# Kernel optimization log

Hardware: AMD Instinct MI355X
Metric: run time of the kernel (lower is better)

The kernel has to match this reference:

```python
import jax, jax.numpy as jnp
import numpy as np

B, T, D, H = 512, 200, 128, 128


def setup_inputs() -> dict:
    key = jax.random.key(0)
    ks = jax.random.split(key, 16)
    r = lambda k, shp, s=0.05: jax.random.normal(k, shp, dtype=jnp.float32) * s
    F = 3 * D + H  # concat([item_eb, his_sum, item_eb*his_sum, final_state2])
    return {
        "item_eb": jax.random.normal(ks[0], (B, D), dtype=jnp.float32),
        "item_his_eb": jax.random.normal(ks[1], (B, T, D), dtype=jnp.float32),
        "Wg1": r(ks[2], (D + H, 2 * H)), "bg1": jnp.ones((2 * H,), jnp.float32),
        "Wc1": r(ks[3], (D + H, H)), "bc1": jnp.zeros((H,), jnp.float32),
        "att_w1": r(ks[4], (4 * H, 80)), "att_b1": jnp.zeros((80,), jnp.float32),
        "att_w2": r(ks[5], (80, 40)), "att_b2": jnp.zeros((40,), jnp.float32),
        "att_w3": r(ks[6], (40, 1)), "att_b3": jnp.zeros((1,), jnp.float32),
        "Wg2": r(ks[7], (2 * H, 2 * H)), "bg2": jnp.ones((2 * H,), jnp.float32),
        "Wc2": r(ks[8], (2 * H, H)), "bc2": jnp.zeros((H,), jnp.float32),
        "fc1_w": r(ks[9], (F, 200)), "fc1_b": jnp.zeros((200,), jnp.float32),
        "alpha1": jnp.full((200,), 0.25, jnp.float32),
        "fc2_w": r(ks[10], (200, 80)), "fc2_b": jnp.zeros((80,), jnp.float32),
        "alpha2": jnp.full((80,), 0.25, jnp.float32),
        "fc3_w": r(ks[11], (80, 2)), "fc3_b": jnp.zeros((2,), jnp.float32),
        "seq_len": jax.random.randint(ks[12], (B,), 1, T + 1).astype(jnp.int32),
    }


def _gru_scan(x_btd, Wg, bg, Wc, bc, seq_len, att=None):
    """GRU (TF GRUCell math) or AUGRU if att [B,T] is given.
    Honors sequence_length semantics of tf dynamic_rnn: state copied through,
    outputs zeroed past each row's length."""
    Bx, Tx, _ = x_btd.shape
    Hh = Wc.shape[1]
    xs = jnp.swapaxes(x_btd, 0, 1)  # [T,B,Din]
    ts = jnp.arange(Tx)
    a_ts = jnp.swapaxes(att, 0, 1) if att is not None else jnp.zeros((Tx, Bx), x_btd.dtype)
    h0 = jnp.zeros((Bx, Hh), x_btd.dtype)

    def step(h, xat):
        x, a, t = xat
        gates = jax.nn.sigmoid(jnp.concatenate([x, h], axis=-1) @ Wg + bg)
        rg, u = jnp.split(gates, 2, axis=-1)
        c = jnp.tanh(jnp.concatenate([x, rg * h], axis=-1) @ Wc + bc)
        if att is not None:  # VecAttGRUCell: u = (1 - att_score) * u
            u = (1.0 - a[:, None]) * u
        hn = u * h + (1.0 - u) * c
        valid = (t < seq_len)[:, None]
        hn = jnp.where(valid, hn, h)
        out = jnp.where(valid, hn, jnp.zeros_like(hn))
        return hn, out

    hT, outs = jax.lax.scan(step, h0, (xs, a_ts, ts))
    return jnp.swapaxes(outs, 0, 1), hT  # [B,T,H], [B,H]


def _forward(item_eb, item_his_eb, Wg1, bg1, Wc1, bc1, att_w1, att_b1, att_w2, att_b2,
             att_w3, att_b3, Wg2, bg2, Wc2, bc2, fc1_w, fc1_b, alpha1, fc2_w, fc2_b,
             alpha2, fc3_w, fc3_b, seq_len):
    Bx, Tx, Dx = item_his_eb.shape
    mask = jnp.arange(Tx)[None, :] < seq_len[:, None]  # [B,T] bool
    # rnn_1: plain GRU over history embeddings
    rnn1, _ = _gru_scan(item_his_eb, Wg1, bg1, Wc1, bc1, seq_len)
    # din_fcn_attention: concat trick + 3-layer scorer + masked softmax
    q = jnp.broadcast_to(item_eb[:, None, :], rnn1.shape)
    din_all = jnp.concatenate([q, rnn1, q - rnn1, q * rnn1], axis=-1)  # [B,T,4H]
    h1 = jax.nn.sigmoid(din_all @ att_w1 + att_b1)
    h2 = jax.nn.sigmoid(h1 @ att_w2 + att_b2)
    scores = (h2 @ att_w3 + att_b3)[..., 0]  # [B,T]
    NEG_INF = jnp.float32(-(2.0 ** 32) + 1.0)  # DIEN padding value
    scores = jnp.where(mask, scores, NEG_INF)
    alphas = jax.nn.softmax(scores, axis=-1)  # [B,T]
    # rnn_2: AUGRU (VecAttGRUCell) gated by attention scores; take final state
    _, final_state2 = _gru_scan(rnn1, Wg2, bg2, Wc2, bc2, seq_len, att=alphas)
    # fcn head on concatenated features
    his_sum = jnp.sum(item_his_eb * mask[..., None].astype(item_his_eb.dtype), axis=1)
    feat = jnp.concatenate([item_eb, his_sum, item_eb * his_sum, final_state2], axis=-1)
    prelu = lambda x, a: jnp.maximum(x, 0.0) + a * jnp.minimum(x, 0.0)
    z = prelu(feat @ fc1_w + fc1_b, alpha1)
    z = prelu(z @ fc2_w + fc2_b, alpha2)
    logits = z @ fc3_w + fc3_b  # [B,2]
    return jax.nn.softmax(logits, axis=-1)


def reference(item_eb, item_his_eb, Wg1, bg1, Wc1, bc1, att_w1, att_b1, att_w2, att_b2,
              att_w3, att_b3, Wg2, bg2, Wc2, bc2, fc1_w, fc1_b, alpha1, fc2_w, fc2_b,
              alpha2, fc3_w, fc3_b, seq_len):
    return _forward(item_eb, item_his_eb, Wg1, bg1, Wc1, bc1, att_w1, att_b1, att_w2,
                    att_b2, att_w3, att_b3, Wg2, bg2, Wc2, bc2, fc1_w, fc1_b, alpha1,
                    fc2_w, fc2_b, alpha2, fc3_w, fc3_b, seq_len)
```

## Files before the change

### kernel.cpp

```cpp
#include <hip/hip_runtime.h>
#include <hip/hip_bf16.h>


typedef __attribute__((ext_vector_type(8))) short bf16x8;
typedef __attribute__((ext_vector_type(4))) float f32x4;
typedef _Float16 f16x2 __attribute__((ext_vector_type(2)));

#define NC 4
#define TC 50
#define CROWS 25600
#define CSH 3276800

static __device__ __forceinline__ unsigned short f2bf(float f) {
  union { __hip_bfloat16 h; unsigned short u; } v;
  v.h = __float2bfloat16(f);
  return v.u;
}
static __device__ __forceinline__ float bf2f(unsigned short u) {
  union { __hip_bfloat16 h; unsigned short u; } v;
  v.u = u;
  return __bfloat162float(v.h);
}
static __device__ __forceinline__ unsigned short f2h(float f) {
  union { _Float16 h; unsigned short u; } v;
  v.h = (_Float16)f;
  return v.u;
}
static __device__ __forceinline__ float h2f(unsigned short u) {
  union { unsigned short u; _Float16 h; } v;
  v.u = u;
  return (float)v.h;
}
static __device__ __forceinline__ unsigned int pkf16(float a, float b) {
  union { f16x2 v; unsigned int u; } c;
  c.v = (f16x2){(_Float16)a, (_Float16)b};
  return c.u;
}
static __device__ __forceinline__ void dot2a(float& acc, unsigned int w, unsigned int h) {
  asm volatile("v_dot2_f32_f16 %0, %1, %2, %0" : "+v"(acc) : "v"(w), "v"(h));
}
static __device__ __forceinline__ void gbar() {
  __builtin_amdgcn_sched_barrier(0);
  asm volatile("s_waitcnt lgkmcnt(0)" ::: "memory");
  __builtin_amdgcn_s_barrier();
  __builtin_amdgcn_sched_barrier(0);
}

__global__ __launch_bounds__(256) void prep_weights(
    const float* __restrict__ item_eb,
    const float* __restrict__ Wg1, const float* __restrict__ Wc1,
    const float* __restrict__ Wg2, const float* __restrict__ Wc2,
    const float* __restrict__ aw1, const float* __restrict__ aw2,
    const float* __restrict__ aw3,
    const float* __restrict__ bg1, const float* __restrict__ bc1,
    const float* __restrict__ bg2, const float* __restrict__ bc2,
    const float* __restrict__ ab1, const float* __restrict__ ab2,
    unsigned short* __restrict__ W1xT, unsigned short* __restrict__ W2xT,
    unsigned short* __restrict__ AW1T, unsigned short* __restrict__ AW2T,
    float* __restrict__ b384_1, float* __restrict__ b384_2,
    float* __restrict__ bA1, float* __restrict__ bA2,
    unsigned int* __restrict__ WgP1, unsigned int* __restrict__ WcP1,
    unsigned int* __restrict__ WgP2, unsigned int* __restrict__ WcP2,
    float* __restrict__ w3p, unsigned short* __restrict__ Xq,
    float* __restrict__ hstate)
{
  int e = blockIdx.x * 256 + threadIdx.x;
  if (e < 49152) {
    int n = e >> 7, k = e & 127;
    float v1 = (n < 256) ? Wg1[k * 256 + n] : Wc1[k * 128 + (n - 256)];
    float v2 = (n < 256) ? Wg2[k * 256 + n] : Wc2[k * 128 + (n - 256)];
    W1xT[e] = f2bf(v1);
    W2xT[e] = f2bf(v2);
  }
  if (e < 65536) {
    int n = e >> 9, k = e & 511;
    AW1T[e] = f2bf(n < 80 ? aw1[k * 80 + n] : 0.f);
    Xq[e] = f2bf(item_eb[e]);
    hstate[e] = 0.f;
  }
  if (e < 16384) {
    int n = e >> 7, k = e & 127;
    AW2T[e] = f2bf((n < 40 && k < 80) ? aw2[k * 40 + n] : 0.f);
  }
  if (e < 16384) {
    int i = e >> 8, tt = e & 255;
    int row = 128 + 2 * i;
    WgP1[e] = pkf16(Wg1[row * 256 + tt], Wg1[(row + 1) * 256 + tt]);
    WgP2[e] = pkf16(Wg2[row * 256 + tt], Wg2[(row + 1) * 256 + tt]);
  }
  if (e < 8192) {
    int i = e >> 8, tt = e & 255;
    int jc = tt >> 1, half = tt & 1;
    int row = 128 + half * 64 + 2 * i;
    WcP1[e] = pkf16(Wc1[row * 128 + jc], Wc1[(row + 1) * 128 + jc]);
    WcP2[e] = pkf16(Wc2[row * 128 + jc], Wc2[(row + 1) * 128 + jc]);
  }
  if (e < 384) {
    b384_1[e] = (e < 256) ? bg1[e] : bc1[e - 256];
    b384_2[e] = (e < 256) ? bg2[e] : bc2[e - 256];
  }
  if (e < 128) {
    bA1[e] = (e < 80) ? ab1[e] : 0.f;
    bA2[e] = (e < 40) ? ab2[e] : 0.f;
    w3p[e] = (e < 40) ? aw3[e] : 0.f;
  }
}

__global__ __launch_bounds__(256) void cast_his_t(const float4* __restrict__ in4,
                                                  ushort4* __restrict__ out4)
{
  int i = blockIdx.x * 256 + threadIdx.x;
  float4 v = in4[i];
  int d4 = (i & 31) << 2;
  int bt = i >> 5;
  int tt = bt % 200, bb = bt / 200;
  out4[(((size_t)tt * 512 + bb) * 128 + d4) >> 2] =
      make_ushort4(f2bf(v.x), f2bf(v.y), f2bf(v.z), f2bf(v.w));
}

struct GemmP {
  const unsigned short* A;
  const unsigned short* B;
  const float* bias;
  unsigned short* out;
  float* scores;
  const float* w3p;
  const float* b3;
  const unsigned short* Xq;
  const unsigned short* rnn1;
  long rowbase;
  int K, ldc, mtiles, tbase;
};

static __device__ __forceinline__ uint4 bfop(uint4 q, uint4 r, bool mul) {
  unsigned short* qs = (unsigned short*)&q;
  unsigned short* rs = (unsigned short*)&r;
  uint4 o;
  unsigned short* os = (unsigned short*)&o;
#pragma unroll
  for (int i = 0; i < 8; i++) {
    float a = bf2f(qs[i]), b = bf2f(rs[i]);
    os[i] = f2bf(mul ? a * b : a - b);
  }
  return o;
}

template <int SRC, int EPI>
__device__ __forceinline__ void gemm_body(const GemmP& P, int tile, char* smem) {
// ... 64 lines not shown
  if (EPI == 2) {
    float sp[2][4] = {{0.f, 0.f, 0.f, 0.f}, {0.f, 0.f, 0.f, 0.f}};
#pragma unroll
    for (int n = 0; n < 8; n++) {
      int gcol = n * 16 + lcol;
      float bb = P.bias[gcol];
      float w3 = P.w3p[gcol];
#pragma unroll
      for (int m = 0; m < 2; m++)
#pragma unroll
        for (int i = 0; i < 4; i++) {
          float v = acc[m][n][i] + bb;
          sp[m][i] += w3 / (1.f + __expf(-v));
        }
    }
#pragma unroll
    for (int msk = 1; msk < 16; msk <<= 1)
#pragma unroll
      for (int m = 0; m < 2; m++)
#pragma unroll
        for (int i = 0; i < 4; i++) sp[m][i] += __shfl_xor(sp[m][i], msk);
    float b3v = P.b3[0];
    if (lcol == 0) {
#pragma unroll
      for (int m = 0; m < 2; m++)
#pragma unroll
        for (int i = 0; i < 4; i++) {
          long grow = mBase + w * 32 + m * 16 + lrow4 + i;
          int b = (int)(grow & 511);
          int tp = (int)(grow >> 9) + P.tbase;
          P.scores[b * 200 + tp] = sp[m][i] + b3v;
        }
    }
  } else {
#pragma unroll
    for (int n = 0; n < 8; n++) {
      int gcol = nBase + n * 16 + lcol;
      float bb = P.bias[gcol];
#pragma unroll
      for (int m = 0; m < 2; m++)
#pragma unroll
        for (int i = 0; i < 4; i++) {
          long grow = mBase + w * 32 + m * 16 + lrow4 + i;
          float v = acc[m][n][i] + bb;
          if (EPI == 0) P.out[grow * P.ldc + gcol] = f2h(v);
          else          P.out[grow * P.ldc + gcol] = f2bf(1.f / (1.f + __expf(-v)));
        }
    }
  }
}

struct GruP {
  const unsigned short* xproj;
  const unsigned int* WgP;
  const unsigned int* WcP;
  const int* seqlen;
  const float* alphas;
  unsigned short* outbf;
  float* hstate;
  int tbase;
};

template <int AUGRU>
__device__ void gru_body(const GruP& P, int r, char* smem) {
  float* hF = (float*)smem;
  float* uF = hF + 128;
  unsigned int* hH = (unsigned int*)(uF + 128);
  unsigned int* rghP = hH + 64;
  const int t = threadIdx.x;
  const int jc = t >> 1;
  const int len = P.seqlen[r];
  int nsteps = len - P.tbase;
  if (nsteps > TC) nsteps = TC;

  if (nsteps <= 0) {
    if (!AUGRU && t < 64) {
      for (int s = 0; s < TC; s++)
        ((unsigned int*)(P.outbf + ((size_t)(P.tbase + s) * 512 + r) * 128))[t] = 0;
    }
    return;
  }
  __builtin_amdgcn_s_setprio(1);

  unsigned int wg[64], wc[32];
#pragma unroll
  for (int i = 0; i < 64; i++) wg[i] = P.WgP[i * 256 + t];
#pragma unroll
  for (int i = 0; i < 32; i++) wc[i] = P.WcP[i * 256 + t];

  if (t < 128) hF[t] = P.hstate[r * 128 + t];
  if (t < 64) hH[t] = pkf16(P.hstate[r * 128 + 2 * t], P.hstate[r * 128 + 2 * t + 1]);
  gbar();

  const unsigned short* xp = P.xproj;
  const size_t RS = (size_t)512 * 384;
  const size_t base = (size_t)r * 384;
  unsigned short gA = xp[base + t], cA = xp[base + 256 + jc];
  int s1 = nsteps > 1 ? 1 : 0;
  unsigned short gB = xp[s1 * RS + base + t], cB = xp[s1 * RS + base + 256 + jc];
  float alA = AUGRU ? P.alphas[r * 200 + P.tbase] : 0.f;
  float alB = AUGRU ? P.alphas[r * 200 + P.tbase + s1] : 0.f;

  for (int ts = 0; ts < nsteps; ++ts) {
    int tsn = (ts + 2 < nsteps) ? ts + 2 : nsteps - 1;
    size_t off = (size_t)tsn * RS + base;
    unsigned short gC = xp[off + t];
    unsigned short cC = xp[off + 256 + jc];
    float alC = AUGRU ? P.alphas[r * 200 + P.tbase + tsn] : 0.f;

    float a0 = 0.f, a1 = 0.f, a2 = 0.f, a3 = 0.f;
#pragma unroll
    for (int q = 0; q < 4; q++) {
      uint4 h0 = *(const uint4*)&hH[q * 16 + 0];
      uint4 h1 = *(const uint4*)&hH[q * 16 + 4];
      uint4 h2 = *(const uint4*)&hH[q * 16 + 8];
      uint4 h3 = *(const uint4*)&hH[q * 16 + 12];
      dot2a(a0, wg[q * 16 + 0], h0.x);  dot2a(a1, wg[q * 16 + 1], h0.y);
      dot2a(a2, wg[q * 16 + 2], h0.z);  dot2a(a3, wg[q * 16 + 3], h0.w);
      dot2a(a0, wg[q * 16 + 4], h1.x);  dot2a(a1, wg[q * 16 + 5], h1.y);
      dot2a(a2, wg[q * 16 + 6], h1.z);  dot2a(a3, wg[q * 16 + 7], h1.w);
      dot2a(a0, wg[q * 16 + 8], h2.x);  dot2a(a1, wg[q * 16 + 9], h2.y);
      dot2a(a2, wg[q * 16 + 10], h2.z); dot2a(a3, wg[q * 16 + 11], h2.w);
      dot2a(a0, wg[q * 16 + 12], h3.x); dot2a(a1, wg[q * 16 + 13], h3.y);
      dot2a(a2, wg[q * 16 + 14], h3.z); dot2a(a3, wg[q * 16 + 15], h3.w);
    }
    float a = (a0 + a1) + (a2 + a3) + h2f(gA);
    float g = 1.f / (1.f + __expf(-a));
    if (t < 128) {
      float rgh = g * hF[t];
      float rh2 = __shfl_down(rgh, 1);
      if (!(t & 1)) rghP[t >> 1] = pkf16(rgh, rh2);
    } else {
      uF[t - 128] = g;
    }
    gbar();

    float c0 = 0.f, c1 = 0.f;
    const uint4* rp = (const uint4*)&rghP[(t & 1) * 32];
#pragma unroll
    for (int q = 0; q < 8; q++) {
      uint4 rq = rp[q];
      dot2a(c0, wc[q * 4 + 0], rq.x);
      dot2a(c1, wc[q * 4 + 1], rq.y);
      dot2a(c0, wc[q * 4 + 2], rq.z);
      dot2a(c1, wc[q * 4 + 3], rq.w);
    }
    float c = c0 + c1;
    c += __shfl_xor(c, 1);
    c += h2f(cA);
    c = fminf(fmaxf(c, -15.f), 15.f);
    float e2 = __expf(2.f * c);
    c = 1.f - 2.f / (e2 + 1.f);
    float u = uF[jc];
    if (AUGRU) u *= (1.f - alA);
    float h = hF[jc];
    float hn = u * h + (1.f - u) * c;
    float hnHi = __shfl_down(hn, 2);
    if (!(t & 1)) {
      hF[jc] = hn;
      if (!AUGRU) P.outbf[((size_t)(P.tbase + ts) * 512 + r) * 128 + jc] = f2bf(hn);
    }
    if (!(t & 3)) hH[t >> 2] = pkf16(hn, hnHi);
    gbar();

    gA = gB; cA = cB; alA = alB;
    gB = gC; cB = cC; alB = alC;
  }

  if (t < 128) P.hstate[r * 128 + t] = hF[t];
  if (!AUGRU && nsteps < TC && t < 64) {
    for (int s = nsteps; s < TC; s++)
      ((unsigned int*)(P.outbf + ((size_t)(P.tbase + s) * 512 + r) * 128))[t] = 0;
  }
}

__device__ void hsum_body(const float* __restrict__ his, float* __restrict__ hs,
                          const int* __restrict__ seqlen, int b, char* smem) {
  float* sm = (float*)smem;
  int t = threadIdx.x;
  int len = seqlen[b];
  int col = t & 127, hf = t >> 7;
  float s = 0.f;
  for (int ts = hf; ts < len; ts += 2) s += his[((size_t)b * 200 + ts) * 128 + col];
  sm[t] = s;
  __syncthreads();
  if (t < 128) hs[b * 128 + t] = sm[t] + sm[t + 128];
}

template <int AUG, int GRU, int S1, int E1, int S2, int E2, int S3, int E3, int HS>
__global__ __launch_bounds__(256) void fatk(GruP gp, GemmP p1, int c1,
                                            GemmP p2, int c2, GemmP p3,
                                            const float* hisp, float* hsp)
{
  extern __shared__ char smem[];
  int id = blockIdx.x;
  if constexpr (GRU) {
    if (id < 512) { gru_body<AUG>(gp, id, smem); return; }
    id -= 512;
  }
  if constexpr (HS) {
    if (id < 512) { hsum_body(hisp, hsp, gp.seqlen, id, smem); return; }
    id -= 512;
  }
  if constexpr (S1 >= 0) {
    if (id < c1) { gemm_body<S1, E1>(p1, id, smem); return; }
    id -= c1;
  }
  if constexpr (S2 >= 0) {
    if (id < c2) { gemm_body<S2, E2>(p2, id, smem); return; }
    id -= c2;
  }
  if constexpr (S3 >= 0) gemm_body<S3, E3>(p3, id, smem);
}

__global__ __launch_bounds__(256) void mask_softmax(
    const float* __restrict__ scores, const int* __restrict__ seqlen,
    float* __restrict__ alphas, float* __restrict__ hstate)
{
  int b = blockIdx.x, t = threadIdx.x;
  __shared__ float red[256];
  if (t < 128) hstate[b * 128 + t] = 0.f;
  int len = seqlen[b];
  float s = (t < 200 && t < len) ? scores[b * 200 + t] : -1e30f;
  red[t] = s;
  __syncthreads();
  for (int o = 128; o > 0; o >>= 1) {
    if (t < o) red[t] = fmaxf(red[t], red[t + o]);
    __syncthreads();
  }
  float m = red[0];
  __syncthreads();
  float e = (t < 200 && t < len) ? __expf(s - m) : 0.f;
  red[t] = e;
  __syncthreads();
  for (int o = 128; o > 0; o >>= 1) {
    if (t < o) red[t] += red[t + o];
    __syncthreads();
  }
  float denom = red[0];
  if (t < 200) alphas[b * 200 + t] = e / denom;
}

__global__ __launch_bounds__(256) void head_kernel(
    const float* __restrict__ item_eb, const float* __restrict__ hs,
    const float* __restrict__ hstate,
    const float* __restrict__ w1, const float* __restrict__ b1, const float* __restrict__ a1,
    const float* __restrict__ w2, const float* __restrict__ b2, const float* __restrict__ a2,
    const float* __restrict__ w3, const float* __restrict__ b3,
    float* __restrict__ out)
{
  int b = blockIdx.x, t = threadIdx.x;
// ... 25 lines not shown
  __syncthreads();
  if (t == 0) {
    float l0 = b3[0], l1 = b3[1];
    for (int k = 0; k < 80; k++) {
      float z = z2[k];
      l0 += z * w3[k * 2];
      l1 += z * w3[k * 2 + 1];
    }
    float m = fmaxf(l0, l1);
    float e0 = __expf(l0 - m), e1 = __expf(l1 - m);
    out[b * 2 + 0] = e0 / (e0 + e1);
    out[b * 2 + 1] = e1 / (e0 + e1);
  }
}

extern "C" void kernel_launch(void* const* d_in, const int* in_sizes, int n_in,
                              void* d_out, int out_size, void* d_ws, size_t ws_size,
                              hipStream_t stream)
{
  const float* item_eb = (const float*)d_in[0];
  const float* his     = (const float*)d_in[1];
  const float* Wg1     = (const float*)d_in[2];
  const float* bg1     = (const float*)d_in[3];
  const float* Wc1     = (const float*)d_in[4];
  const float* bc1     = (const float*)d_in[5];
  const float* aw1     = (const float*)d_in[6];
  const float* ab1     = (const float*)d_in[7];
  const float* aw2     = (const float*)d_in[8];
  const float* ab2     = (const float*)d_in[9];
  const float* aw3     = (const float*)d_in[10];
  const float* ab3     = (const float*)d_in[11];
  const float* Wg2     = (const float*)d_in[12];
  const float* bg2     = (const float*)d_in[13];
  const float* Wc2     = (const float*)d_in[14];
  const float* bc2     = (const float*)d_in[15];
  const float* fc1w    = (const float*)d_in[16];
  const float* fc1b    = (const float*)d_in[17];
  const float* al1     = (const float*)d_in[18];
  const float* fc2w    = (const float*)d_in[19];
  const float* fc2b    = (const float*)d_in[20];
  const float* al2     = (const float*)d_in[21];
  const float* fc3w    = (const float*)d_in[22];
  const float* fc3b    = (const float*)d_in[23];
  const int*   seqlen  = (const int*)d_in[24];

  char* ws = (char*)d_ws;
  unsigned short* XhA    = (unsigned short*)(ws + 0L);
  unsigned short* xpA    = (unsigned short*)(ws + 26214400L);
  unsigned short* xpB    = (unsigned short*)(ws + 45875200L);
  unsigned short* rnn1   = (unsigned short*)(ws + 65536000L);
  float*          scores = (float*)(ws + 91750400L);
  float*          alphas = (float*)(ws + 92160000L);
  float*          hstate = (float*)(ws + 92569600L);
  unsigned int*   WgP1   = (unsigned int*)(ws + 92831744L);
  unsigned int*   WcP1   = (unsigned int*)(ws + 92897280L);
  unsigned int*   WgP2   = (unsigned int*)(ws + 92930048L);
  unsigned int*   WcP2   = (unsigned int*)(ws + 92995584L);
  unsigned short* W1xT   = (unsigned short*)(ws + 93028352L);
  unsigned short* W2xT   = (unsigned short*)(ws + 93126656L);
  unsigned short* AW1T   = (unsigned short*)(ws + 93224960L);
  unsigned short* AW2T   = (unsigned short*)(ws + 93356032L);
  float*          b384_1 = (float*)(ws + 93388800L);
  float*          b384_2 = (float*)(ws + 93390336L);
  float*          bA1    = (float*)(ws + 93391872L);
  float*          bA2    = (float*)(ws + 93392384L);
  float*          w3p    = (float*)(ws + 93392896L);
  unsigned short* Xq     = (unsigned short*)(ws + 93393408L);
  float*          hs     = scores;

  unsigned short* h1[NC] = {XhA, XhA + CSH, XhA + 2 * CSH, XhA + 3 * CSH};

  const int SM = 32768;
  GruP gz{}; GemmP dz{};
  gz.seqlen = seqlen;

  auto mkGru = [&](int c, int aug) {
    GruP g;
    g.xproj = (c & 1) ? xpB : xpA;
    g.WgP = aug ? WgP2 : WgP1; g.WcP = aug ? WcP2 : WcP1;
    g.seqlen = seqlen; g.alphas = alphas;
    g.outbf = aug ? nullptr : rnn1; g.hstate = hstate; g.tbase = c * TC;
    return g;
  };
  auto mkXp = [&](const unsigned short* A, const float* bias, unsigned short* outp) {
    GemmP p{}; p.A = A; p.B = (bias == b384_1) ? W1xT : W2xT; p.bias = bias;
    p.out = outp; p.K = 128; p.ldc = 384; p.mtiles = 200; return p;
  };
  auto mkAtt1 = [&](int c) {
    GemmP p{}; p.B = AW1T; p.bias = bA1; p.out = h1[c];
    p.Xq = Xq; p.rnn1 = rnn1; p.rowbase = (long)c * CROWS;
    p.K = 512; p.ldc = 128; p.mtiles = 200; return p;
  };
  auto mkAtt2 = [&](int c) {
    GemmP p{}; p.A = h1[c]; p.B = AW2T; p.bias = bA2;
    p.scores = scores; p.w3p = w3p; p.b3 = ab3;
    p.K = 128; p.ldc = 128; p.mtiles = 200; p.tbase = c * TC; return p;
  };

  prep_weights<<<256, 256, 0, stream>>>(item_eb, Wg1, Wc1, Wg2, Wc2, aw1, aw2, aw3,
                                        bg1, bc1, bg2, bc2, ab1, ab2,
                                        W1xT, W2xT, AW1T, AW2T, b384_1, b384_2, bA1, bA2,
                                        WgP1, WcP1, WgP2, WcP2, w3p, Xq, hstate);
  cast_his_t<<<12800, 256, 0, stream>>>((const float4*)his, (ushort4*)XhA);

  fatk<0,0, 0,0, -1,0, -1,0, 0><<<600, 256, SM, stream>>>(
      gz, mkXp(XhA, b384_1, xpA), 600, dz, 0, dz, nullptr, nullptr);
  fatk<0,1, 0,0, -1,0, -1,0, 0><<<1112, 256, SM, stream>>>(
      mkGru(0,0), mkXp(XhA + (size_t)CSH, b384_1, xpB), 600, dz, 0, dz, nullptr, nullptr);
  fatk<0,1, 0,0, -1,0, -1,0, 0><<<1112, 256, SM, stream>>>(
      mkGru(1,0), mkXp(XhA + (size_t)2*CSH, b384_1, xpA), 600, dz, 0, dz, nullptr, nullptr);
  fatk<0,1, 0,0, 1,1, -1,0, 0><<<1712, 256, SM, stream>>>(
      mkGru(2,0), mkXp(XhA + (size_t)3*CSH, b384_1, xpB), 600, mkAtt1(0), 200, dz, nullptr, nullptr);
  fatk<0,1, 1,1, 0,2, -1,0, 0><<<912, 256, SM, stream>>>(
      mkGru(3,0), mkAtt1(1), 200, mkAtt2(0), 200, dz, nullptr, nullptr);
  fatk<0,0, 1,1, 0,2, 0,0, 0><<<1000, 256, SM, stream>>>(
      gz, mkAtt1(2), 200, mkAtt2(1), 200, mkXp(rnn1, b384_2, xpA), nullptr, nullptr);
  fatk<0,0, 1,1, 0,2, 0,0, 0><<<1000, 256, SM, stream>>>(
      gz, mkAtt1(3), 200, mkAtt2(2), 200, mkXp(rnn1 + (size_t)CSH, b384_2, xpB), nullptr, nullptr);
  fatk<0,0, 0,2, -1,0, -1,0, 0><<<200, 256, SM, stream>>>(
      gz, mkAtt2(3), 200, dz, 0, dz, nullptr, nullptr);
  mask_softmax<<<512, 256, 0, stream>>>(scores, seqlen, alphas, hstate);
  fatk<1,1, -1,0, -1,0, -1,0, 1><<<1024, 256, SM, stream>>>(
      mkGru(0,1), dz, 0, dz, 0, dz, his, hs);
  fatk<1,1, 0,0, -1,0, -1,0, 0><<<1112, 256, SM, stream>>>(
      mkGru(1,1), mkXp(rnn1 + (size_t)2*CSH, b384_2, xpA), 600, dz, 0, dz, nullptr, nullptr);
  fatk<1,1, 0,0, -1,0, -1,0, 0><<<1112, 256, SM, stream>>>(
      mkGru(2,1), mkXp(rnn1 + (size_t)3*CSH, b384_2, xpB), 600, dz, 0, dz, nullptr, nullptr);
  fatk<1,1, -1,0, -1,0, -1,0, 0><<<512, 256, SM, stream>>>(
      mkGru(3,1), dz, 0, dz, 0, dz, nullptr, nullptr);
  head_kernel<<<512, 256, 0, stream>>>(item_eb, hs, hstate,
                                       fc1w, fc1b, al1, fc2w, fc2b, al2,
                                       fc3w, fc3b, (float*)d_out);
}
```

Measured before the change: 664.2 us.

## Batch GRU recurrence 16 rows per block using f16 MFMA instead of dot2

Replaces the per-row GRU blocks (512 blocks, each doing one hidden-state matvec with v_dot2 and registers-held packed weights) with 32 blocks that each process 16 batch rows, computing the h·W gate and candidate products with 16x16x32 f16 MFMA from a swizzled LDS tile. Weights are re-laid out as transposed f16 matrices. Sequence-length masking moves to per-row select inside a block that runs to the max length of its 16 rows. This cuts the number of GRU workgroups and their weight-register loading, freeing CUs for the fused GEMM work. The cost is serialized per-step latency concentrated in only 32 blocks and wasted steps for shorter rows.

```diff
diff --git a/kernel.cpp b/kernel.cpp
--- a/kernel.cpp
+++ b/kernel.cpp
@@ -4,12 +4,13 @@
 
 typedef __attribute__((ext_vector_type(8))) short bf16x8;
 typedef __attribute__((ext_vector_type(4))) float f32x4;
-typedef _Float16 f16x2 __attribute__((ext_vector_type(2)));
+typedef _Float16 f16x8 __attribute__((ext_vector_type(8)));
 
 #define NC 4
 #define TC 50
 #define CROWS 25600
 #define CSH 3276800
+#define NGRU 32
 
 static __device__ __forceinline__ unsigned short f2bf(float f) {
   union { __hip_bfloat16 h; unsigned short u; } v;
@@ -30,14 +31,6 @@
   union { unsigned short u; _Float16 h; } v;
   v.u = u;
   return (float)v.h;
-}
-static __device__ __forceinline__ unsigned int pkf16(float a, float b) {
-  union { f16x2 v; unsigned int u; } c;
-  c.v = (f16x2){(_Float16)a, (_Float16)b};
-  return c.u;
-}
-static __device__ __forceinline__ void dot2a(float& acc, unsigned int w, unsigned int h) {
-  asm volatile("v_dot2_f32_f16 %0, %1, %2, %0" : "+v"(acc) : "v"(w), "v"(h));
 }
 static __device__ __forceinline__ void gbar() {
   __builtin_amdgcn_sched_barrier(0);
@@ -59,8 +52,8 @@
     unsigned short* __restrict__ AW1T, unsigned short* __restrict__ AW2T,
     float* __restrict__ b384_1, float* __restrict__ b384_2,
     float* __restrict__ bA1, float* __restrict__ bA2,
-    unsigned int* __restrict__ WgP1, unsigned int* __restrict__ WcP1,
-    unsigned int* __restrict__ WgP2, unsigned int* __restrict__ WcP2,
+    unsigned short* __restrict__ WghT1, unsigned short* __restrict__ WchT1,
+    unsigned short* __restrict__ WghT2, unsigned short* __restrict__ WchT2,
     float* __restrict__ w3p, unsigned short* __restrict__ Xq,
     float* __restrict__ hstate)
 {
@@ -82,18 +75,15 @@
     int n = e >> 7, k = e & 127;
     AW2T[e] = f2bf((n < 40 && k < 80) ? aw2[k * 40 + n] : 0.f);
   }
+  if (e < 32768) {
+    int n = e >> 7, k = e & 127;
+    WghT1[e] = f2h(Wg1[(128 + k) * 256 + n]);
+    WghT2[e] = f2h(Wg2[(128 + k) * 256 + n]);
+  }
   if (e < 16384) {
-    int i = e >> 8, tt = e & 255;
-    int row = 128 + 2 * i;
-    WgP1[e] = pkf16(Wg1[row * 256 + tt], Wg1[(row + 1) * 256 + tt]);
-    WgP2[e] = pkf16(Wg2[row * 256 + tt], Wg2[(row + 1) * 256 + tt]);
-  }
-  if (e < 8192) {
-    int i = e >> 8, tt = e & 255;
-    int jc = tt >> 1, half = tt & 1;
-    int row = 128 + half * 64 + 2 * i;
-    WcP1[e] = pkf16(Wc1[row * 128 + jc], Wc1[(row + 1) * 128 + jc]);
-    WcP2[e] = pkf16(Wc2[row * 128 + jc], Wc2[(row + 1) * 128 + jc]);
+    int n = e >> 7, k = e & 127;
+    WchT1[e] = f2h(Wc1[(128 + k) * 128 + n]);
+    WchT2[e] = f2h(Wc2[(128 + k) * 128 + n]);
   }
   if (e < 384) {
     b384_1[e] = (e < 256) ? bg1[e] : bc1[e - 256];
@@ -264,8 +254,8 @@
 
 struct GruP {
   const unsigned short* xproj;
-  const unsigned int* WgP;
-  const unsigned int* WcP;
+  const unsigned short* Wgh;
+  const unsigned short* Wch;
   const int* seqlen;
   const float* alphas;
   unsigned short* outbf;
@@ -273,116 +263,161 @@
   int tbase;
 };
 
+static __device__ __forceinline__ int swz(int row, int colByte) {
+  return row * 256 + (colByte ^ ((row & 7) << 4));
+}
+
 template <int AUGRU>
-__device__ void gru_body(const GruP& P, int r, char* smem) {
-  float* hF = (float*)smem;
-  float* uF = hF + 128;
-  unsigned int* hH = (unsigned int*)(uF + 128);
-  unsigned int* rghP = hH + 64;
+__device__ void gru_body(const GruP& P, int rblk, char* smem) {
   const int t = threadIdx.x;
-  const int jc = t >> 1;
-  const int len = P.seqlen[r];
-  int nsteps = len - P.tbase;
-  if (nsteps > TC) nsteps = TC;
-
-  if (nsteps <= 0) {
-    if (!AUGRU && t < 64) {
-      for (int s = 0; s < TC; s++)
-        ((unsigned int*)(P.outbf + ((size_t)(P.tbase + s) * 512 + r) * 128))[t] = 0;
+  const int w = t >> 6, l = t & 63;
+  const int lo = l & 15, hi = l >> 4;
+  const int b0 = rblk * 16;
+
+  int mlen = 0;
+#pragma unroll
+  for (int i = 0; i < 16; i++) mlen = max(mlen, P.seqlen[b0 + i]);
+  int bsteps = mlen - P.tbase;
+  if (bsteps > TC) bsteps = TC;
+
+  if (bsteps <= 0) {
+    if (!AUGRU) {
+      for (int s = 0; s < TC; s++) {
+        unsigned int* zp = (unsigned int*)(P.outbf + ((size_t)(P.tbase + s) * 512 + b0) * 128);
+        for (int e = t; e < 1024; e += 256) zp[e] = 0;
+      }
     }
     return;
   }
   __builtin_amdgcn_s_setprio(1);
 
-  unsigned int wg[64], wc[32];
-#pragma unroll
-  for (int i = 0; i < 64; i++) wg[i] = P.WgP[i * 256 + t];
-#pragma unroll
-  for (int i = 0; i < 32; i++) wc[i] = P.WcP[i * 256 + t];
-
-  if (t < 128) hF[t] = P.hstate[r * 128 + t];
-  if (t < 64) hH[t] = pkf16(P.hstate[r * 128 + 2 * t], P.hstate[r * 128 + 2 * t + 1]);
+  int len[4];
+#pragma unroll
+  for (int i = 0; i < 4; i++) len[i] = P.seqlen[b0 + hi * 4 + i];
+
+  f16x8 wg[4][4], wc[2][4];
+#pragma unroll
+  for (int n = 0; n < 4; n++) {
+    int nt = w + n * 4;
+#pragma unroll
+    for (int ck = 0; ck < 4; ck++)
+      wg[n][ck] = *(const f16x8*)(P.Wgh + (nt * 16 + lo) * 128 + ck * 32 + hi * 8);
+  }
+#pragma unroll
+  for (int n = 0; n < 2; n++) {
+    int nt = w + n * 4;
+#pragma unroll
+    for (int ck = 0; ck < 4; ck++)
+      wc[n][ck] = *(const f16x8*)(P.Wch + (nt * 16 + lo) * 128 + ck * 32 + hi * 8);
+  }
+
+  char* hL = smem;
+  char* rL = smem + 4096;
+
+  const int colc0 = w * 16 + lo, colc1 = 64 + w * 16 + lo;
+  float hreg[2][4];
+#pragma unroll
+  for (int i = 0; i < 4; i++) {
+    int row = hi * 4 + i;
+    float h0 = P.hstate[(b0 + row) * 128 + colc0];
+    float h1 = P.hstate[(b0 + row) * 128 + colc1];
+    hreg[0][i] = h0;
+    hreg[1][i] = h1;
+    *(unsigned short*)(hL + swz(row, colc0 * 2)) = f2h(h0);
+    *(unsigned short*)(hL + swz(row, colc1 * 2)) = f2h(h1);
+  }
   gbar();
 
   const unsigned short* xp = P.xproj;
   const size_t RS = (size_t)512 * 384;
-  const size_t base = (size_t)r * 384;
-  unsigned short gA = xp[base + t], cA = xp[base + 256 + jc];
-  int s1 = nsteps > 1 ? 1 : 0;
-  unsigned short gB = xp[s1 * RS + base + t], cB = xp[s1 * RS + base + 256 + jc];
-  float alA = AUGRU ? P.alphas[r * 200 + P.tbase] : 0.f;
-  float alB = AUGRU ? P.alphas[r * 200 + P.tbase + s1] : 0.f;
-
-  for (int ts = 0; ts < nsteps; ++ts) {
-    int tsn = (ts + 2 < nsteps) ? ts + 2 : nsteps - 1;
-    size_t off = (size_t)tsn * RS + base;
-    unsigned short gC = xp[off + t];
-    unsigned short cC = xp[off + 256 + jc];
-    float alC = AUGRU ? P.alphas[r * 200 + P.tbase + tsn] : 0.f;
-
-    float a0 = 0.f, a1 = 0.f, a2 = 0.f, a3 = 0.f;
-#pragma unroll
-    for (int q = 0; q < 4; q++) {
-      uint4 h0 = *(const uint4*)&hH[q * 16 + 0];
-      uint4 h1 = *(const uint4*)&hH[q * 16 + 4];
-      uint4 h2 = *(const uint4*)&hH[q * 16 + 8];
-      uint4 h3 = *(const uint4*)&hH[q * 16 + 12];
-      dot2a(a0, wg[q * 16 + 0], h0.x);  dot2a(a1, wg[q * 16 + 1], h0.y);
-      dot2a(a2, wg[q * 16 + 2], h0.z);  dot2a(a3, wg[q * 16 + 3], h0.w);
-      dot2a(a0, wg[q * 16 + 4], h1.x);  dot2a(a1, wg[q * 16 + 5], h1.y);
-      dot2a(a2, wg[q * 16 + 6], h1.z);  dot2a(a3, wg[q * 16 + 7], h1.w);
-      dot2a(a0, wg[q * 16 + 8], h2.x);  dot2a(a1, wg[q * 16 + 9], h2.y);
-      dot2a(a2, wg[q * 16 + 10], h2.z); dot2a(a3, wg[q * 16 + 11], h2.w);
-      dot2a(a0, wg[q * 16 + 12], h3.x); dot2a(a1, wg[q * 16 + 13], h3.y);
-      dot2a(a2, wg[q * 16 + 14], h3.z); dot2a(a3, wg[q * 16 + 15], h3.w);
-    }
-    float a = (a0 + a1) + (a2 + a3) + h2f(gA);
-    float g = 1.f / (1.f + __expf(-a));
-    if (t < 128) {
-      float rgh = g * hF[t];
-      float rh2 = __shfl_down(rgh, 1);
-      if (!(t & 1)) rghP[t >> 1] = pkf16(rgh, rh2);
-    } else {
-      uF[t - 128] = g;
+
+  for (int ts = 0; ts < bsteps; ++ts) {
+    unsigned short xgs[4][4], xcs[2][4];
+    float al[4];
+#pragma unroll
+    for (int i = 0; i < 4; i++) {
+      size_t rb = (size_t)ts * RS + (size_t)(b0 + hi * 4 + i) * 384;
+      xgs[0][i] = xp[rb + 16 * w + lo];
+      xgs[1][i] = xp[rb + 64 + 16 * w + lo];
+      xgs[2][i] = xp[rb + 128 + 16 * w + lo];
+      xgs[3][i] = xp[rb + 192 + 16 * w + lo];
+      xcs[0][i] = xp[rb + 256 + 16 * w + lo];
+      xcs[1][i] = xp[rb + 320 + 16 * w + lo];
+      if (AUGRU) al[i] = P.alphas[(b0 + hi * 4 + i) * 200 + P.tbase + ts];
+    }
+
+    f16x8 aF[4];
+#pragma unroll
+    for (int ck = 0; ck < 4; ck++)
+      aF[ck] = *(const f16x8*)(hL + swz(lo, ck * 64 + hi * 16));
+    f32x4 acc1[4];
+#pragma unroll
+    for (int n = 0; n < 4; n++) {
+      acc1[n] = 0.f;
+#pragma unroll
+      for (int ck = 0; ck < 4; ck++)
+        acc1[n] = __builtin_amdgcn_mfma_f32_16x16x32_f16(aF[ck], wg[n][ck], acc1[n], 0, 0, 0);
+    }
+    float uu[2][4];
+#pragma unroll
+    for (int i = 0; i < 4; i++) {
+      int row = hi * 4 + i;
+      float r0 = 1.f / (1.f + __expf(-(acc1[0][i] + h2f(xgs[0][i]))));
+      float r1 = 1.f / (1.f + __expf(-(acc1[1][i] + h2f(xgs[1][i]))));
+      *(unsigned short*)(rL + swz(row, colc0 * 2)) = f2h(r0 * hreg[0][i]);
+      *(unsigned short*)(rL + swz(row, colc1 * 2)) = f2h(r1 * hreg[1][i]);
+      uu[0][i] = 1.f / (1.f + __expf(-(acc1[2][i] + h2f(xgs[2][i]))));
+      uu[1][i] = 1.f / (1.f + __expf(-(acc1[3][i] + h2f(xgs[3][i]))));
     }
     gbar();
 
-    float c0 = 0.f, c1 = 0.f;
-    const uint4* rp = (const uint4*)&rghP[(t & 1) * 32];
-#pragma unroll
-    for (int q = 0; q < 8; q++) {
-      uint4 rq = rp[q];
-      dot2a(c0, wc[q * 4 + 0], rq.x);
-      dot2a(c1, wc[q * 4 + 1], rq.y);
-      dot2a(c0, wc[q * 4 + 2], rq.z);
-      dot2a(c1, wc[q * 4 + 3], rq.w);
-    }
-    float c = c0 + c1;
-    c += __shfl_xor(c, 1);
-    c += h2f(cA);
-    c = fminf(fmaxf(c, -15.f), 15.f);
-    float e2 = __expf(2.f * c);
-    c = 1.f - 2.f / (e2 + 1.f);
-    float u = uF[jc];
-    if (AUGRU) u *= (1.f - alA);
-    float h = hF[jc];
-    float hn = u * h + (1.f - u) * c;
-    float hnHi = __shfl_down(hn, 2);
-    if (!(t & 1)) {
-      hF[jc] = hn;
-      if (!AUGRU) P.outbf[((size_t)(P.tbase + ts) * 512 + r) * 128 + jc] = f2bf(hn);
-    }
-    if (!(t & 3)) hH[t >> 2] = pkf16(hn, hnHi);
+    f16x8 rF[4];
+#pragma unroll
+    for (int ck = 0; ck < 4; ck++)
+      rF[ck] = *(const f16x8*)(rL + swz(lo, ck * 64 + hi * 16));
+    f32x4 acc2[2];
+#pragma unroll
+    for (int n = 0; n < 2; n++) {
+      acc2[n] = 0.f;
+#pragma unroll
+      for (int ck = 0; ck < 4; ck++)
+        acc2[n] = __builtin_amdgcn_mfma_f32_16x16x32_f16(rF[ck], wc[n][ck], acc2[n], 0, 0, 0);
+    }
+#pragma unroll
+    for (int i = 0; i < 4; i++) {
+      int row = hi * 4 + i;
+      bool valid = (P.tbase + ts) < len[i];
+#pragma unroll
+      for (int j = 0; j < 2; j++) {
+        int col = j ? colc1 : colc0;
+        float c = acc2[j][i] + h2f(xcs[j][i]);
+        c = fminf(fmaxf(c, -15.f), 15.f);
+        float e2 = __expf(2.f * c);
+        c = 1.f - 2.f / (e2 + 1.f);
+        float u = uu[j][i];
+        if (AUGRU) u *= (1.f - al[i]);
+        float hn = u * hreg[j][i] + (1.f - u) * c;
+        hn = valid ? hn : hreg[j][i];
+        hreg[j][i] = hn;
+        *(unsigned short*)(hL + swz(row, col * 2)) = f2h(hn);
+        if (!AUGRU)
+          P.outbf[((size_t)(P.tbase + ts) * 512 + b0 + row) * 128 + col] =
+              valid ? f2bf(hn) : (unsigned short)0;
+      }
+    }
     gbar();
-
-    gA = gB; cA = cB; alA = alB;
-    gB = gC; cB = cC; alB = alC;
-  }
-
-  if (t < 128) P.hstate[r * 128 + t] = hF[t];
-  if (!AUGRU && nsteps < TC && t < 64) {
-    for (int s = nsteps; s < TC; s++)
-      ((unsigned int*)(P.outbf + ((size_t)(P.tbase + s) * 512 + r) * 128))[t] = 0;
+  }
+
+#pragma unroll
+  for (int i = 0; i < 4; i++) {
+    P.hstate[(b0 + hi * 4 + i) * 128 + colc0] = hreg[0][i];
+    P.hstate[(b0 + hi * 4 + i) * 128 + colc1] = hreg[1][i];
+  }
+  if (!AUGRU) {
+    for (int s = bsteps; s < TC; s++) {
+      unsigned int* zp = (unsigned int*)(P.outbf + ((size_t)(P.tbase + s) * 512 + b0) * 128);
+      for (int e = t; e < 1024; e += 256) zp[e] = 0;
+    }
   }
 }
 
@@ -407,8 +442,8 @@
   extern __shared__ char smem[];
   int id = blockIdx.x;
   if constexpr (GRU) {
-    if (id < 512) { gru_body<AUG>(gp, id, smem); return; }
-    id -= 512;
+    if (id < NGRU) { gru_body<AUG>(gp, id, smem); return; }
+    id -= NGRU;
   }
   if constexpr (HS) {
     if (id < 512) { hsum_body(hisp, hsp, gp.seqlen, id, smem); return; }
@@ -540,10 +575,10 @@
   float*          scores = (float*)(ws + 91750400L);
   float*          alphas = (float*)(ws + 92160000L);
   float*          hstate = (float*)(ws + 92569600L);
-  unsigned int*   WgP1   = (unsigned int*)(ws + 92831744L);
-  unsigned int*   WcP1   = (unsigned int*)(ws + 92897280L);
-  unsigned int*   WgP2   = (unsigned int*)(ws + 92930048L);
-  unsigned int*   WcP2   = (unsigned int*)(ws + 92995584L);
+  unsigned short* WghT1  = (unsigned short*)(ws + 92831744L);
+  unsigned short* WchT1  = (unsigned short*)(ws + 92897280L);
+  unsigned short* WghT2  = (unsigned short*)(ws + 92930048L);
+  unsigned short* WchT2  = (unsigned short*)(ws + 92995584L);
   unsigned short* W1xT   = (unsigned short*)(ws + 93028352L);
   unsigned short* W2xT   = (unsigned short*)(ws + 93126656L);
   unsigned short* AW1T   = (unsigned short*)(ws + 93224960L);
@@ -565,7 +600,8 @@
   auto mkGru = [&](int c, int aug) {
     GruP g;
     g.xproj = (c & 1) ? xpB : xpA;
-    g.WgP = aug ? WgP2 : WgP1; g.WcP = aug ? WcP2 : WcP1;
+    g.Wgh = aug ? WghT2 : WghT1;
+    g.Wch = aug ? WchT2 : WchT1;
     g.seqlen = seqlen; g.alphas = alphas;
     g.outbf = aug ? nullptr : rnn1; g.hstate = hstate; g.tbase = c * TC;
     return g;
@@ -588,18 +624,18 @@
   prep_weights<<<256, 256, 0, stream>>>(item_eb, Wg1, Wc1, Wg2, Wc2, aw1, aw2, aw3,
                                         bg1, bc1, bg2, bc2, ab1, ab2,
                                         W1xT, W2xT, AW1T, AW2T, b384_1, b384_2, bA1, bA2,
-                                        WgP1, WcP1, WgP2, WcP2, w3p, Xq, hstate);
+                                        WghT1, WchT1, WghT2, WchT2, w3p, Xq, hstate);
   cast_his_t<<<12800, 256, 0, stream>>>((const float4*)his, (ushort4*)XhA);
 
   fatk<0,0, 0,0, -1,0, -1,0, 0><<<600, 256, SM, stream>>>(
       gz, mkXp(XhA, b384_1, xpA), 600, dz, 0, dz, nullptr, nullptr);
-  fatk<0,1, 0,0, -1,0, -1,0, 0><<<1112, 256, SM, stream>>>(
+  fatk<0,1, 0,0, -1,0, -1,0, 0><<<632, 256, SM, stream>>>(
       mkGru(0,0), mkXp(XhA + (size_t)CSH, b384_1, xpB), 600, dz, 0, dz, nullptr, nullptr);
-  fatk<0,1, 0,0, -1,0, -1,0, 0><<<1112, 256, SM, stream>>>(
+  fatk<0,1, 0,0, -1,0, -1,0, 0><<<632, 256, SM, stream>>>(
       mkGru(1,0), mkXp(XhA + (size_t)2*CSH, b384_1, xpA), 600, dz, 0, dz, nullptr, nullptr);
-  fatk<0,1, 0,0, 1,1, -1,0, 0><<<1712, 256, SM, stream>>>(
+  fatk<0,1, 0,0, 1,1, -1,0, 0><<<832, 256, SM, stream>>>(
       mkGru(2,0), mkXp(XhA + (size_t)3*CSH, b384_1, xpB), 600, mkAtt1(0), 200, dz, nullptr, nullptr);
-  fatk<0,1, 1,1, 0,2, -1,0, 0><<<912, 256, SM, stream>>>(
+  fatk<0,1, 1,1, 0,2, -1,0, 0><<<432, 256, SM, stream>>>(
       mkGru(3,0), mkAtt1(1), 200, mkAtt2(0), 200, dz, nullptr, nullptr);
   fatk<0,0, 1,1, 0,2, 0,0, 0><<<1000, 256, SM, stream>>>(
       gz, mkAtt1(2), 200, mkAtt2(1), 200, mkXp(rnn1, b384_2, xpA), nullptr, nullptr);
@@ -608,13 +644,13 @@
   fatk<0,0, 0,2, -1,0, -1,0, 0><<<200, 256, SM, stream>>>(
       gz, mkAtt2(3), 200, dz, 0, dz, nullptr, nullptr);
   mask_softmax<<<512, 256, 0, stream>>>(scores, seqlen, alphas, hstate);
-  fatk<1,1, -1,0, -1,0, -1,0, 1><<<1024, 256, SM, stream>>>(
+  fatk<1,1, -1,0, -1,0, -1,0, 1><<<544, 256, SM, stream>>>(
       mkGru(0,1), dz, 0, dz, 0, dz, his, hs);
-  fatk<1,1, 0,0, -1,0, -1,0, 0><<<1112, 256, SM, stream>>>(
+  fatk<1,1, 0,0, -1,0, -1,0, 0><<<632, 256, SM, stream>>>(
       mkGru(1,1), mkXp(rnn1 + (size_t)2*CSH, b384_2, xpA), 600, dz, 0, dz, nullptr, nullptr);
-  fatk<1,1, 0,0, -1,0, -1,0, 0><<<1112, 256, SM, stream>>>(
+  fatk<1,1, 0,0, -1,0, -1,0, 0><<<632, 256, SM, stream>>>(
       mkGru(2,1), mkXp(rnn1 + (size_t)3*CSH, b384_2, xpB), 600, dz, 0, dz, nullptr, nullptr);
-  fatk<1,1, -1,0, -1,0, -1,0, 0><<<512, 256, SM, stream>>>(
+  fatk<1,1, -1,0, -1,0, -1,0, 0><<<NGRU, 256, SM, stream>>>(
       mkGru(3,1), dz, 0, dz, 0, dz, nullptr, nullptr);
   head_kernel<<<512, 256, 0, stream>>>(item_eb, hs, hstate,
                                        fc1w, fc1b, al1, fc2w, fc2b, al2,
```

Measured after the change: 945.2 us. 42.3% more time.

## Process two batch rows per GRU block to reuse register-resident weights

Applied to the files above, without the earlier changes.

Each GRU workgroup now advances two sequences at once, sharing the per-thread gate and candidate weight registers across both rows. GRU block count is halved and the fused launch sizes shrink to match. Steps past each row's length are masked, so state is carried and outputs are zeroed while the block runs to the longer of the two lengths. This halves weight loads and barrier-bound blocks per row but roughly doubles per-step work inside the serial chain, and a block with two unequal lengths does extra work.

```diff
diff --git a/kernel.cpp b/kernel.cpp
--- a/kernel.cpp
+++ b/kernel.cpp
@@ -274,21 +274,27 @@
 };
 
 template <int AUGRU>
-__device__ void gru_body(const GruP& P, int r, char* smem) {
-  float* hF = (float*)smem;
-  float* uF = hF + 128;
-  unsigned int* hH = (unsigned int*)(uF + 128);
-  unsigned int* rghP = hH + 64;
+__device__ void gru_body(const GruP& P, int rblk, char* smem) {
+  float* hFa = (float*)smem;
+  float* hFb = hFa + 128;
+  float* uFa = hFb + 128;
+  float* uFb = uFa + 128;
+  unsigned short* hHa = (unsigned short*)(uFb + 128);
+  unsigned short* hHb = hHa + 128;
+  unsigned short* rgA = hHb + 128;
+  unsigned short* rgB = rgA + 128;
   const int t = threadIdx.x;
-  const int jc = t >> 1;
-  const int len = P.seqlen[r];
-  int nsteps = len - P.tbase;
-  if (nsteps > TC) nsteps = TC;
-
-  if (nsteps <= 0) {
-    if (!AUGRU && t < 64) {
+  const int jc = t >> 1, half = t & 1;
+  const int rA = rblk * 2, rB = rA + 1;
+  const int lenA = P.seqlen[rA], lenB = P.seqlen[rB];
+  int nsA = lenA - P.tbase; if (nsA > TC) nsA = TC;
+  int nsB = lenB - P.tbase; if (nsB > TC) nsB = TC;
+  int bsteps = nsA > nsB ? nsA : nsB;
+
+  if (bsteps <= 0) {
+    if (!AUGRU && t < 128) {
       for (int s = 0; s < TC; s++)
-        ((unsigned int*)(P.outbf + ((size_t)(P.tbase + s) * 512 + r) * 128))[t] = 0;
+        ((unsigned int*)(P.outbf + ((size_t)(P.tbase + s) * 512 + rA) * 128))[t] = 0;
     }
     return;
   }
@@ -300,33 +306,42 @@
 #pragma unroll
   for (int i = 0; i < 32; i++) wc[i] = P.WcP[i * 256 + t];
 
-  if (t < 128) hF[t] = P.hstate[r * 128 + t];
-  if (t < 64) hH[t] = pkf16(P.hstate[r * 128 + 2 * t], P.hstate[r * 128 + 2 * t + 1]);
+  if (t < 128) {
+    float ha = P.hstate[rA * 128 + t], hb = P.hstate[rB * 128 + t];
+    hFa[t] = ha; hFb[t] = hb;
+    hHa[t] = f2h(ha); hHb[t] = f2h(hb);
+  }
   gbar();
 
   const unsigned short* xp = P.xproj;
   const size_t RS = (size_t)512 * 384;
-  const size_t base = (size_t)r * 384;
-  unsigned short gA = xp[base + t], cA = xp[base + 256 + jc];
-  int s1 = nsteps > 1 ? 1 : 0;
-  unsigned short gB = xp[s1 * RS + base + t], cB = xp[s1 * RS + base + 256 + jc];
-  float alA = AUGRU ? P.alphas[r * 200 + P.tbase] : 0.f;
-  float alB = AUGRU ? P.alphas[r * 200 + P.tbase + s1] : 0.f;
-
-  for (int ts = 0; ts < nsteps; ++ts) {
-    int tsn = (ts + 2 < nsteps) ? ts + 2 : nsteps - 1;
-    size_t off = (size_t)tsn * RS + base;
-    unsigned short gC = xp[off + t];
-    unsigned short cC = xp[off + 256 + jc];
-    float alC = AUGRU ? P.alphas[r * 200 + P.tbase + tsn] : 0.f;
+  const size_t baA = (size_t)rA * 384, baB = (size_t)rB * 384;
+  unsigned short xgA0 = xp[baA + t], xcA0 = xp[baA + 256 + jc];
+  unsigned short xgB0 = xp[baB + t], xcB0 = xp[baB + 256 + jc];
+  int s1 = bsteps > 1 ? 1 : 0;
+  unsigned short xgA1 = xp[s1 * RS + baA + t], xcA1 = xp[s1 * RS + baA + 256 + jc];
+  unsigned short xgB1 = xp[s1 * RS + baB + t], xcB1 = xp[s1 * RS + baB + 256 + jc];
+  float alA0 = AUGRU ? P.alphas[rA * 200 + P.tbase] : 0.f;
+  float alB0 = AUGRU ? P.alphas[rB * 200 + P.tbase] : 0.f;
+  float alA1 = AUGRU ? P.alphas[rA * 200 + P.tbase + s1] : 0.f;
+  float alB1 = AUGRU ? P.alphas[rB * 200 + P.tbase + s1] : 0.f;
+
+  for (int ts = 0; ts < bsteps; ++ts) {
+    int tsn = (ts + 2 < bsteps) ? ts + 2 : bsteps - 1;
+    size_t offA = (size_t)tsn * RS + baA, offB = (size_t)tsn * RS + baB;
+    unsigned short xgAn = xp[offA + t], xcAn = xp[offA + 256 + jc];
+    unsigned short xgBn = xp[offB + t], xcBn = xp[offB + 256 + jc];
+    float alAn = AUGRU ? P.alphas[rA * 200 + P.tbase + tsn] : 0.f;
+    float alBn = AUGRU ? P.alphas[rB * 200 + P.tbase + tsn] : 0.f;
 
     float a0 = 0.f, a1 = 0.f, a2 = 0.f, a3 = 0.f;
+    float b0 = 0.f, b1 = 0.f, b2 = 0.f, b3 = 0.f;
+    const uint4* ha4 = (const uint4*)hHa;
+    const uint4* hb4 = (const uint4*)hHb;
 #pragma unroll
     for (int q = 0; q < 4; q++) {
-      uint4 h0 = *(const uint4*)&hH[q * 16 + 0];
-      uint4 h1 = *(const uint4*)&hH[q * 16 + 4];
-      uint4 h2 = *(const uint4*)&hH[q * 16 + 8];
-      uint4 h3 = *(const uint4*)&hH[q * 16 + 12];
+      uint4 h0 = ha4[q * 4 + 0], h1 = ha4[q * 4 + 1];
+      uint4 h2 = ha4[q * 4 + 2], h3 = ha4[q * 4 + 3];
       dot2a(a0, wg[q * 16 + 0], h0.x);  dot2a(a1, wg[q * 16 + 1], h0.y);
       dot2a(a2, wg[q * 16 + 2], h0.z);  dot2a(a3, wg[q * 16 + 3], h0.w);
       dot2a(a0, wg[q * 16 + 4], h1.x);  dot2a(a1, wg[q * 16 + 5], h1.y);
@@ -335,54 +350,86 @@
       dot2a(a2, wg[q * 16 + 10], h2.z); dot2a(a3, wg[q * 16 + 11], h2.w);
       dot2a(a0, wg[q * 16 + 12], h3.x); dot2a(a1, wg[q * 16 + 13], h3.y);
       dot2a(a2, wg[q * 16 + 14], h3.z); dot2a(a3, wg[q * 16 + 15], h3.w);
-    }
-    float a = (a0 + a1) + (a2 + a3) + h2f(gA);
-    float g = 1.f / (1.f + __expf(-a));
+      uint4 k0 = hb4[q * 4 + 0], k1 = hb4[q * 4 + 1];
+      uint4 k2 = hb4[q * 4 + 2], k3 = hb4[q * 4 + 3];
+      dot2a(b0, wg[q * 16 + 0], k0.x);  dot2a(b1, wg[q * 16 + 1], k0.y);
+      dot2a(b2, wg[q * 16 + 2], k0.z);  dot2a(b3, wg[q * 16 + 3], k0.w);
+      dot2a(b0, wg[q * 16 + 4], k1.x);  dot2a(b1, wg[q * 16 + 5], k1.y);
+      dot2a(b2, wg[q * 16 + 6], k1.z);  dot2a(b3, wg[q * 16 + 7], k1.w);
+      dot2a(b0, wg[q * 16 + 8], k2.x);  dot2a(b1, wg[q * 16 + 9], k2.y);
+      dot2a(b2, wg[q * 16 + 10], k2.z); dot2a(b3, wg[q * 16 + 11], k2.w);
+      dot2a(b0, wg[q * 16 + 12], k3.x); dot2a(b1, wg[q * 16 + 13], k3.y);
+      dot2a(b2, wg[q * 16 + 14], k3.z); dot2a(b3, wg[q * 16 + 15], k3.w);
+    }
+    float aA = (a0 + a1) + (a2 + a3) + h2f(xgA0);
+    float aB = (b0 + b1) + (b2 + b3) + h2f(xgB0);
+    float gA = 1.f / (1.f + __expf(-aA));
+    float gB = 1.f / (1.f + __expf(-aB));
     if (t < 128) {
-      float rgh = g * hF[t];
-      float rh2 = __shfl_down(rgh, 1);
-      if (!(t & 1)) rghP[t >> 1] = pkf16(rgh, rh2);
+      rgA[t] = f2h(gA * hFa[t]);
+      rgB[t] = f2h(gB * hFb[t]);
     } else {
-      uF[t - 128] = g;
+      uFa[t - 128] = gA;
+      uFb[t - 128] = gB;
     }
     gbar();
 
-    float c0 = 0.f, c1 = 0.f;
-    const uint4* rp = (const uint4*)&rghP[(t & 1) * 32];
+    float cA0f = 0.f, cA1f = 0.f, cB0f = 0.f, cB1f = 0.f;
+    const uint4* ra4 = (const uint4*)rgA + half * 8;
+    const uint4* rb4 = (const uint4*)rgB + half * 8;
 #pragma unroll
     for (int q = 0; q < 8; q++) {
-      uint4 rq = rp[q];
-      dot2a(c0, wc[q * 4 + 0], rq.x);
-      dot2a(c1, wc[q * 4 + 1], rq.y);
-      dot2a(c0, wc[q * 4 + 2], rq.z);
-      dot2a(c1, wc[q * 4 + 3], rq.w);
-    }
-    float c = c0 + c1;
-    c += __shfl_xor(c, 1);
-    c += h2f(cA);
-    c = fminf(fmaxf(c, -15.f), 15.f);
-    float e2 = __expf(2.f * c);
-    c = 1.f - 2.f / (e2 + 1.f);
-    float u = uF[jc];
-    if (AUGRU) u *= (1.f - alA);
-    float h = hF[jc];
-    float hn = u * h + (1.f - u) * c;
-    float hnHi = __shfl_down(hn, 2);
-    if (!(t & 1)) {
-      hF[jc] = hn;
-      if (!AUGRU) P.outbf[((size_t)(P.tbase + ts) * 512 + r) * 128 + jc] = f2bf(hn);
-    }
-    if (!(t & 3)) hH[t >> 2] = pkf16(hn, hnHi);
+      uint4 rq = ra4[q];
+      dot2a(cA0f, wc[q * 4 + 0], rq.x);
+      dot2a(cA1f, wc[q * 4 + 1], rq.y);
+      dot2a(cA0f, wc[q * 4 + 2], rq.z);
+      dot2a(cA1f, wc[q * 4 + 3], rq.w);
+      uint4 sq = rb4[q];
+      dot2a(cB0f, wc[q * 4 + 0], sq.x);
+      dot2a(cB1f, wc[q * 4 + 1], sq.y);
+      dot2a(cB0f, wc[q * 4 + 2], sq.z);
+      dot2a(cB1f, wc[q * 4 + 3], sq.w);
+    }
+    float cA = cA0f + cA1f;
+    float cB = cB0f + cB1f;
+    cA += __shfl_xor(cA, 1);
+    cB += __shfl_xor(cB, 1);
+    cA += h2f(xcA0);
+    cB += h2f(xcB0);
+    cA = fminf(fmaxf(cA, -15.f), 15.f);
+    cB = fminf(fmaxf(cB, -15.f), 15.f);
+    float eA = __expf(2.f * cA), eB = __expf(2.f * cB);
+    cA = 1.f - 2.f / (eA + 1.f);
+    cB = 1.f - 2.f / (eB + 1.f);
+    float uA = uFa[jc], uB = uFb[jc];
+    if (AUGRU) { uA *= (1.f - alA0); uB *= (1.f - alB0); }
+    float hA = hFa[jc], hB = hFb[jc];
+    float hnA = uA * hA + (1.f - uA) * cA;
+    float hnB = uB * hB + (1.f - uB) * cB;
+    bool vA = (P.tbase + ts) < lenA, vB = (P.tbase + ts) < lenB;
+    hnA = vA ? hnA : hA;
+    hnB = vB ? hnB : hB;
+    if (!half) {
+      hFa[jc] = hnA; hFb[jc] = hnB;
+      hHa[jc] = f2h(hnA); hHb[jc] = f2h(hnB);
+      if (!AUGRU) {
+        P.outbf[((size_t)(P.tbase + ts) * 512 + rA) * 128 + jc] = vA ? f2bf(hnA) : (unsigned short)0;
+        P.outbf[((size_t)(P.tbase + ts) * 512 + rB) * 128 + jc] = vB ? f2bf(hnB) : (unsigned short)0;
+      }
+    }
     gbar();
 
-    gA = gB; cA = cB; alA = alB;
-    gB = gC; cB = cC; alB = alC;
-  }
-
-  if (t < 128) P.hstate[r * 128 + t] = hF[t];
-  if (!AUGRU && nsteps < TC && t < 64) {
-    for (int s = nsteps; s < TC; s++)
-      ((unsigned int*)(P.outbf + ((size_t)(P.tbase + s) * 512 + r) * 128))[t] = 0;
+    xgA0 = xgA1; xcA0 = xcA1; xgB0 = xgB1; xcB0 = xcB1; alA0 = alA1; alB0 = alB1;
+    xgA1 = xgAn; xcA1 = xcAn; xgB1 = xgBn; xcB1 = xcBn; alA1 = alAn; alB1 = alBn;
+  }
+
+  if (t < 128) {
+    P.hstate[rA * 128 + t] = hFa[t];
+    P.hstate[rB * 128 + t] = hFb[t];
+  }
+  if (!AUGRU && t < 128) {
+    for (int s = bsteps; s < TC; s++)
+      ((unsigned int*)(P.outbf + ((size_t)(P.tbase + s) * 512 + rA) * 128))[t] = 0;
   }
 }
 
@@ -407,8 +454,8 @@
   extern __shared__ char smem[];
   int id = blockIdx.x;
   if constexpr (GRU) {
-    if (id < 512) { gru_body<AUG>(gp, id, smem); return; }
-    id -= 512;
+    if (id < 256) { gru_body<AUG>(gp, id, smem); return; }
+    id -= 256;
   }
   if constexpr (HS) {
     if (id < 512) { hsum_body(hisp, hsp, gp.seqlen, id, smem); return; }
@@ -593,13 +640,13 @@
 
   fatk<0,0, 0,0, -1,0, -1,0, 0><<<600, 256, SM, stream>>>(
       gz, mkXp(XhA, b384_1, xpA), 600, dz, 0, dz, nullptr, nullptr);
-  fatk<0,1, 0,0, -1,0, -1,0, 0><<<1112, 256, SM, stream>>>(
+  fatk<0,1, 0,0, -1,0, -1,0, 0><<<856, 256, SM, stream>>>(
       mkGru(0,0), mkXp(XhA + (size_t)CSH, b384_1, xpB), 600, dz, 0, dz, nullptr, nullptr);
-  fatk<0,1, 0,0, -1,0, -1,0, 0><<<1112, 256, SM, stream>>>(
+  fatk<0,1, 0,0, -1,0, -1,0, 0><<<856, 256, SM, stream>>>(
       mkGru(1,0), mkXp(XhA + (size_t)2*CSH, b384_1, xpA), 600, dz, 0, dz, nullptr, nullptr);
-  fatk<0,1, 0,0, 1,1, -1,0, 0><<<1712, 256, SM, stream>>>(
+  fatk<0,1, 0,0, 1,1, -1,0, 0><<<1056, 256, SM, stream>>>(
       mkGru(2,0), mkXp(XhA + (size_t)3*CSH, b384_1, xpB), 600, mkAtt1(0), 200, dz, nullptr, nullptr);
-  fatk<0,1, 1,1, 0,2, -1,0, 0><<<912, 256, SM, stream>>>(
+  fatk<0,1, 1,1, 0,2, -1,0, 0><<<656, 256, SM, stream>>>(
       mkGru(3,0), mkAtt1(1), 200, mkAtt2(0), 200, dz, nullptr, nullptr);
   fatk<0,0, 1,1, 0,2, 0,0, 0><<<1000, 256, SM, stream>>>(
       gz, mkAtt1(2), 200, mkAtt2(1), 200, mkXp(rnn1, b384_2, xpA), nullptr, nullptr);
@@ -608,13 +655,13 @@
   fatk<0,0, 0,2, -1,0, -1,0, 0><<<200, 256, SM, stream>>>(
       gz, mkAtt2(3), 200, dz, 0, dz, nullptr, nullptr);
   mask_softmax<<<512, 256, 0, stream>>>(scores, seqlen, alphas, hstate);
-  fatk<1,1, -1,0, -1,0, -1,0, 1><<<1024, 256, SM, stream>>>(
+  fatk<1,1, -1,0, -1,0, -1,0, 1><<<768, 256, SM, stream>>>(
       mkGru(0,1), dz, 0, dz, 0, dz, his, hs);
-  fatk<1,1, 0,0, -1,0, -1,0, 0><<<1112, 256, SM, stream>>>(
+  fatk<1,1, 0,0, -1,0, -1,0, 0><<<856, 256, SM, stream>>>(
       mkGru(1,1), mkXp(rnn1 + (size_t)2*CSH, b384_2, xpA), 600, dz, 0, dz, nullptr, nullptr);
-  fatk<1,1, 0,0, -1,0, -1,0, 0><<<1112, 256, SM, stream>>>(
+  fatk<1,1, 0,0, -1,0, -1,0, 0><<<856, 256, SM, stream>>>(
       mkGru(2,1), mkXp(rnn1 + (size_t)3*CSH, b384_2, xpB), 600, dz, 0, dz, nullptr, nullptr);
-  fatk<1,1, -1,0, -1,0, -1,0, 0><<<512, 256, SM, stream>>>(
+  fatk<1,1, -1,0, -1,0, -1,0, 0><<<256, 256, SM, stream>>>(
       mkGru(3,1), dz, 0, dz, 0, dz, nullptr, nullptr);
   head_kernel<<<512, 256, 0, stream>>>(item_eb, hs, hstate,
                                        fc1w, fc1b, al1, fc2w, fc2b, al2,
```

Measured after the change: 890.7 us. +34.1%, slower.
